# Kernel optimization log

Measured on AMD Instinct MI355X. Metric: run time of the kernel, lower is better.

Reference implementation:

```python
import jax, jax.numpy as jnp
import numpy as np

SCALES = [2 ** i for i in range(11)]  # init: scales=10 -> [1,2,...,1024]
B, N, C, K = 8, 1024, 256, 4096


def setup_inputs() -> dict:
    key = jax.random.key(0)
    k1, k2, k3 = jax.random.split(key, 3)
    f_BNC = jax.random.normal(k1, (B, N, C), dtype=jnp.float32)
    base = jax.random.normal(k2, (K, C), dtype=jnp.float32)          # orthogonal-init codebook base
    proj_w = jax.random.normal(k3, (C, C), dtype=jnp.float32) / np.float32(np.sqrt(C))  # xavier-ish
    proj_b = jnp.zeros((C,), dtype=jnp.float32)
    return {"f_BNC": f_BNC, "base": base, "proj_w": proj_w, "proj_b": proj_b}


def _linear_interp(x, out_size):
    # x: [B, C, n] -> [B, C, out_size], matches F.interpolate(mode='linear', align_corners=False)
    n = x.shape[-1]
    scale = n / out_size
    src = jnp.maximum((jnp.arange(out_size, dtype=jnp.float32) + 0.5) * scale - 0.5, 0.0)
    i0 = jnp.floor(src).astype(jnp.int32)
    i1 = jnp.minimum(i0 + 1, n - 1)
    w = (src - i0.astype(jnp.float32)).astype(x.dtype)
    return x[..., i0] * (1.0 - w) + x[..., i1] * w


def reference(f_BNC, base, proj_w, proj_b):
    sg = jax.lax.stop_gradient
    # update_embedding(): embedding = proj(base)
    embedding = base @ proj_w.T + proj_b                 # [K, C]
    emb_ng = sg(embedding)
    e_sq = jnp.sum(emb_ng * emb_ng, axis=1)              # [K]

    f_BCN = jnp.transpose(f_BNC, (0, 2, 1))              # [B, C, N]
    f_ng = sg(f_BCN)
    f_rest = f_ng
    f_hat = jnp.zeros_like(f_ng)
    commit = jnp.float32(0.0)
    qlat = jnp.float32(0.0)
    SN = len(SCALES)

    for pn in SCALES:
        # area interpolation == exact mean pooling since N % pn == 0
        rest_BCp = f_rest.reshape(B, C, pn, N // pn).mean(axis=-1)       # [B, C, pn]
        q = jnp.transpose(rest_BCp, (0, 2, 1)).reshape(-1, C)            # [B*pn, C]
        # squared-distance to codebook (gradients never flow through d: argmin only)
        d = jnp.sum(q * q, axis=1, keepdims=True) + e_sq - 2.0 * (q @ emb_ng.T)  # [B*pn, K]
        idx = jnp.argmin(d, axis=1)                                      # [B*pn]
        h_BnC = embedding[idx].reshape(B, pn, C)                         # gather (grad flows to codebook)
        h_BCn = _linear_interp(jnp.transpose(h_BnC, (0, 2, 1)), N)       # [B, C, N]
        f_hat = f_hat + h_BCn
        # residual feeds only argmin at the next scale -> dead gradient path in torch too
        f_rest = f_rest - sg(h_BCn)
        commit = commit + 0.25 * jnp.mean((sg(f_hat) - f_BCN) ** 2)
        qlat = qlat + jnp.mean((f_hat - f_ng) ** 2)

    commit = commit / SN
    qlat = qlat / SN
    # straight-through: f_hat = (f_hat.data - f_no_grad) + f_BCN
    f_out = sg(f_hat) - f_ng + f_BCN
    return (jnp.transpose(f_out, (0, 2, 1)), commit, qlat)
```

## Files before the change

### kernel.cpp

```cpp
#include <hip/hip_runtime.h>
#include <cfloat>

#define BB 8
#define NN 1024
#define CC 256
#define KK 4096
#define SN 11
#define BNC (BB*NN*CC)
#define RMAX 8192

typedef __attribute__((ext_vector_type(8))) _Float16 half8;
typedef __attribute__((ext_vector_type(4))) float f32x4;

__device__ __forceinline__ void split2(float v, ushort& h, ushort& l) {
    union { _Float16 f; ushort u; } a, b;
    a.f = (_Float16)v;
    b.f = (_Float16)(v - (float)a.f);
    h = a.u; l = b.u;
}

__global__ void transpose_pw(const float* __restrict__ pw, float* __restrict__ pwT) {
    int j = blockIdx.x;
    int c = threadIdx.x;
    pwT[j * CC + c] = pw[c * CC + j];
}

__global__ __launch_bounds__(256) void embed_kernel(
    const float* __restrict__ base, const float* __restrict__ pwT,
    const float* __restrict__ pb, float* __restrict__ emb,
    ushort* __restrict__ eh, ushort* __restrict__ el, float* __restrict__ esq) {
    __shared__ float bs[16][CC];
    __shared__ float wpart[16][4];
    int k0 = blockIdx.x * 16;
    int t = threadIdx.x;
    int w = t >> 6, lane = t & 63;
    for (int i = t; i < 16 * CC; i += 256) bs[i >> 8][i & 255] = base[k0 * CC + i];
    __syncthreads();
    float acc[16];
#pragma unroll
    for (int m = 0; m < 16; ++m) acc[m] = 0.f;
    for (int j = 0; j < CC; ++j) {
        float wv = pwT[j * CC + t];
#pragma unroll
        for (int m = 0; m < 16; ++m) acc[m] += bs[m][j] * wv;
    }
    float bias = pb[t];
#pragma unroll
    for (int m = 0; m < 16; ++m) {
        float v = acc[m] + bias;
        int o = (k0 + m) * CC + t;
        emb[o] = v;
        ushort h, l;
        split2(64.f * v, h, l);
        eh[o] = h; el[o] = l;
        float sq = v * v;
#pragma unroll
        for (int d = 1; d < 64; d <<= 1) sq += __shfl_xor(sq, d);
        if (lane == 0) wpart[m][w] = sq;
    }
    __syncthreads();
    if (t < 16) esq[k0 + t] = wpart[t][0] + wpart[t][1] + wpart[t][2] + wpart[t][3];
}

__global__ __launch_bounds__(256) void init_pool16(const float* __restrict__ f,
                                                   float* __restrict__ p16) {
    int blk = blockIdx.x;
    int t = threadIdx.x;
    int c4 = t & 63;
    const float4* src = (const float4*)(f + (size_t)blk * 16 * CC) + c4;
    float4 s = make_float4(0.f, 0.f, 0.f, 0.f);
#pragma unroll
    for (int j = 0; j < 16; ++j) {
        float4 v = src[(size_t)j * 64];
        s.x += v.x; s.y += v.y; s.z += v.z; s.w += v.w;
    }
    ((float4*)(p16 + (size_t)blk * CC))[c4] = s;
}

__global__ __launch_bounds__(256, 4) void dist_small(
    const float* __restrict__ src, const float* __restrict__ emb,
    const float* __restrict__ esq, int R, int g16, int pn, float inv,
    float* __restrict__ pval, int* __restrict__ pidx) {
    __shared__ float qs[32][CC];
    __shared__ float es[64][33];
    int t = threadIdx.x;
    int ws = t >> 6, j = t & 63;
    int k0 = blockIdx.x * 64;
    int r0c = blockIdx.y * 32;
    {
        int row = t >> 3;
        int f4b = (t & 7) * 8;
        int gr = r0c + row;
        float4 a4[8];
#pragma unroll
        for (int ii = 0; ii < 8; ++ii) a4[ii] = make_float4(0.f, 0.f, 0.f, 0.f);
        if (gr < R) {
            int b = gr / pn, p = gr - b * pn;
            const float4* sp = (const float4*)(src + ((size_t)b * 64 + (size_t)p * g16) * CC) + f4b;
            for (int i = 0; i < g16; ++i) {
#pragma unroll
                for (int ii = 0; ii < 8; ++ii) {
                    float4 v = sp[ii];
                    a4[ii].x += v.x; a4[ii].y += v.y; a4[ii].z += v.z; a4[ii].w += v.w;
                }
                sp += 64;
            }
        }
#pragma unroll
        for (int ii = 0; ii < 8; ++ii) {
            a4[ii].x *= inv; a4[ii].y *= inv; a4[ii].z *= inv; a4[ii].w *= inv;
            *(float4*)&qs[row][(f4b + ii) * 4] = a4[ii];
        }
    }
    float acc[8];
#pragma unroll
    for (int ri = 0; ri < 8; ++ri) acc[ri] = 0.f;
    for (int ck = 0; ck < 8; ++ck) {
        __syncthreads();
        {
            int code = t >> 2, cb = (t & 3) * 8;
            float4 v0 = *(const float4*)&emb[(size_t)(k0 + code) * CC + ck * 32 + cb];
            float4 v1 = *(const float4*)&emb[(size_t)(k0 + code) * CC + ck * 32 + cb + 4];
            es[code][cb + 0] = v0.x; es[code][cb + 1] = v0.y;
            es[code][cb + 2] = v0.z; es[code][cb + 3] = v0.w;
            es[code][cb + 4] = v1.x; es[code][cb + 5] = v1.y;
            es[code][cb + 6] = v1.z; es[code][cb + 7] = v1.w;
        }
        __syncthreads();
        for (int c = 0; c < 32; ++c) {
            float ev = es[j][c];
#pragma unroll
            for (int ri = 0; ri < 8; ++ri)
                acc[ri] += qs[ws + 4 * ri][ck * 32 + c] * ev;
        }
    }
    float esv = esq[k0 + j];
#pragma unroll
    for (int ri = 0; ri < 8; ++ri) {
        int r = r0c + ws + 4 * ri;
        if (r >= R) continue;
        float v = esv - 2.f * acc[ri];
        int bi = k0 + j;
#pragma unroll
        for (int d = 1; d < 64; d <<= 1) {
            float ov = __shfl_xor(v, d);
            int oi = __shfl_xor(bi, d);
            if (ov < v || (ov == v && oi < bi)) { v = ov; bi = oi; }
        }
        if (j == 0) {
            pval[(size_t)r * 64 + blockIdx.x] = v;
            pidx[(size_t)r * 64 + blockIdx.x] = bi;
        }
    }
}

__global__ __launch_bounds__(256, 2) void dist_mfma(
    const ushort* __restrict__ qh, const ushort* __restrict__ ql,
    const ushort* __restrict__ eh, const ushort* __restrict__ el,
    const float* __restrict__ esq,
    float* __restrict__ pval, int* __restrict__ pidx) {
    __shared__ ushort tiles[4096 * 8];
    __shared__ float wv[2][128];
    __shared__ int wi[2][128];
    int t = threadIdx.x;
    int w = t >> 6, lane = t & 63;
    int l15 = lane & 15, hi = lane >> 4;
    int wr = w >> 1, wc = w & 1;
    int r0 = blockIdx.x * 128;
    int kb = blockIdx.y;
    int k0 = kb * 128;

    f32x4 acc[4][4];
#pragma unroll
    for (int mi = 0; mi < 4; ++mi)
#pragma unroll
        for (int ni = 0; ni < 4; ++ni) acc[mi][ni] = (f32x4){0.f, 0.f, 0.f, 0.f};

    for (int ck = 0; ck < 4; ++ck) {
        __syncthreads();
#pragma unroll
        for (int it = 0; it < 16; ++it) {
            int s = it * 256 + t;
            const ushort* g;
            if (s < 2048) {
                int a = s >> 10;
                int rem = s & 1023;
                int row = rem >> 3, sr = rem & 7;
                int c = (ck << 6) + ((sr ^ (row & 7)) << 3);
                g = (a ? ql : qh) + (size_t)(r0 + row) * CC + c;
            } else {
                int s2 = s - 2048;
                int b = s2 >> 10;
                int rem = s2 & 1023;
                int kcol = rem >> 3, sr = rem & 7;
                int c = (ck << 6) + ((sr ^ (kcol & 7)) << 3);
                g = (b ? el : eh) + (size_t)(k0 + kcol) * CC + c;
            }
            ushort* lb = &tiles[(size_t)(it * 256 + (w << 6)) * 8];
            __builtin_amdgcn_global_load_lds(
                (const __attribute__((address_space(1))) unsigned int*)g,
                (__attribute__((address_space(3))) unsigned int*)lb, 16, 0, 0);
        }
        __syncthreads();

#pragma unroll
        for (int kk = 0; kk < 2; ++kk) {
            int cs = (kk << 2) + hi;
            half8 bf0[4], bf1[4], af[4];
#pragma unroll
            for (int ni = 0; ni < 4; ++ni) {
                int kcol = (wc << 6) + (ni << 4) + l15;
                int sb = 2048 + (kcol << 3) + (cs ^ (kcol & 7));
                bf0[ni] = *(const half8*)&tiles[sb * 8];
                bf1[ni] = *(const half8*)&tiles[(sb + 1024) * 8];
            }
#pragma unroll
            for (int mi = 0; mi < 4; ++mi) {
                int row = (wr << 6) + (mi << 4) + l15;
                af[mi] = *(const half8*)&tiles[((row << 3) + (cs ^ (row & 7))) * 8];
            }
#pragma unroll
            for (int mi = 0; mi < 4; ++mi)
#pragma unroll
                for (int ni = 0; ni < 4; ++ni)
                    acc[mi][ni] = __builtin_amdgcn_mfma_f32_16x16x32_f16(af[mi], bf0[ni], acc[mi][ni], 0, 0, 0);
#pragma unroll
            for (int mi = 0; mi < 4; ++mi)
#pragma unroll
                for (int ni = 0; ni < 4; ++ni)
                    acc[mi][ni] = __builtin_amdgcn_mfma_f32_16x16x32_f16(af[mi], bf1[ni], acc[mi][ni], 0, 0, 0);
#pragma unroll
            for (int mi = 0; mi < 4; ++mi) {
                int row = (wr << 6) + (mi << 4) + l15;
                af[mi] = *(const half8*)&tiles[(1024 + (row << 3) + (cs ^ (row & 7))) * 8];
            }
#pragma unroll
            for (int mi = 0; mi < 4; ++mi)
#pragma unroll
                for (int ni = 0; ni < 4; ++ni)
                    acc[mi][ni] = __builtin_amdgcn_mfma_f32_16x16x32_f16(af[mi], bf0[ni], acc[mi][ni], 0, 0, 0);
        }
    }

    int cbase = k0 + (wc << 6) + l15;
    float es4[4];
#pragma unroll
    for (int ni = 0; ni < 4; ++ni) es4[ni] = 4096.f * esq[cbase + ni * 16];
#pragma unroll
    for (int mi = 0; mi < 4; ++mi) {
#pragma unroll
        for (int reg = 0; reg < 4; ++reg) {
            float v = es4[0] - 2.f * acc[mi][0][reg];
            int i = cbase;
#pragma unroll
            for (int ni = 1; ni < 4; ++ni) {
                float v1 = es4[ni] - 2.f * acc[mi][ni][reg];
                if (v1 < v) { v = v1; i = cbase + ni * 16; }
            }
#pragma unroll
            for (int d = 1; d < 16; d <<= 1) {
                float ov = __shfl_xor(v, d);
                int oi = __shfl_xor(i, d);
                if (ov < v || (ov == v && oi < i)) { v = ov; i = oi; }
            }
            if (l15 == 0) {
                int row = (wr << 6) + (mi << 4) + (hi << 2) + reg;
                wv[wc][row] = v;
                wi[wc][row] = i;
            }
        }
    }
    __syncthreads();
    if (t < 128) {
        float v = wv[0][t];
        int i = wi[0][t];
        float ov = wv[1][t];
        int oi = wi[1][t];
        if (ov < v || (ov == v && oi < i)) { v = ov; i = oi; }
        pval[(size_t)(r0 + t) * 64 + kb] = v;
        pidx[(size_t)(r0 + t) * 64 + kb] = i;
    }
}

__global__ __launch_bounds__(256) void update_pool(
    const float* __restrict__ emb, const float* __restrict__ pval,
    const int* __restrict__ pidx, const float* __restrict__ rin,
    float* __restrict__ rout, const float* __restrict__ f,
    float* __restrict__ outp, float* __restrict__ parts,
    ushort* __restrict__ qh, ushort* __restrict__ ql,
    float* __restrict__ qf, float* __restrict__ p16u,
    int pn, int gn, int pnn, int ks, int finalflag) {
    int blk = blockIdx.x;
    int b = blk >> 6, n16 = blk & 63;
    int t = threadIdx.x;
    int w = t >> 6, lane = t & 63;
    int n0 = n16 * 16;
    const float scale = (float)pn * (1.0f / 1024.0f);
    float s_lo = (n0 + 0.5f) * scale - 0.5f;
    if (s_lo < 0.f) s_lo = 0.f;
    int r_lo = (int)s_lo;
    float s_hi = (n0 + 15.5f) * scale - 0.5f;
    if (s_hi < 0.f) s_hi = 0.f;
    int r_hi = min((int)s_hi + 1, pn - 1);
    int cnt = r_hi - r_lo + 1;
    __shared__ int sidx[20];
    for (int ri = w; ri < cnt; ri += 4) {
        size_t rowg = (size_t)(b * pn + r_lo + ri) * 64;
        float v = (lane < ks) ? pval[rowg + lane] : FLT_MAX;
        int i = (lane < ks) ? pidx[rowg + lane] : 0x7fffffff;
#pragma unroll
        for (int d = 1; d < 64; d <<= 1) {
            float ov = __shfl_xor(v, d);
            int oi = __shfl_xor(i, d);
            if (ov < v || (ov == v && oi < i)) { v = ov; i = oi; }
        }
        if (lane == 0) sidx[ri] = i;
    }
    __syncthreads();
    __shared__ float4 rlds[16][64];
    __shared__ float wred[4];
    int nsub = t >> 6;
    int c4 = t & 63;
    float sq = 0.f;
#pragma unroll
    for (int jj = 0; jj < 4; ++jj) {
        int j = nsub + 4 * jj;
        int n = n0 + j;
        float s = (n + 0.5f) * scale - 0.5f;
        if (s < 0.f) s = 0.f;
        int i0 = (int)s;
        float wgt = s - (float)i0;
        int i1 = min(i0 + 1, pn - 1);
        int k0 = sidx[i0 - r_lo];
        int k1 = sidx[i1 - r_lo];
        float4 e0 = ((const float4*)(emb + (size_t)k0 * CC))[c4];
        float4 e1 = ((const float4*)(emb + (size_t)k1 * CC))[c4];
        float wm = 1.f - wgt;
        float4 h = make_float4(wm * e0.x + wgt * e1.x, wm * e0.y + wgt * e1.y,
                               wm * e0.z + wgt * e1.z, wm * e0.w + wgt * e1.w);
        size_t o4 = ((size_t)b * NN + n) * 64 + c4;
        float4 rv0 = ((const float4*)rin)[o4];
        float4 rv = make_float4(rv0.x - h.x, rv0.y - h.y, rv0.z - h.z, rv0.w - h.w);
        if (!finalflag) {
            ((float4*)rout)[o4] = rv;
        } else {
            float4 fv = ((const float4*)f)[o4];
            ((float4*)outp)[o4] = make_float4(fv.x - rv.x, fv.y - rv.y,
                                              fv.z - rv.z, fv.w - rv.w);
        }
        sq += rv.x * rv.x + rv.y * rv.y + rv.z * rv.z + rv.w * rv.w;
        rlds[j][c4] = rv;
    }
    for (int off = 32; off > 0; off >>= 1) sq += __shfl_down(sq, off);
    if (lane == 0) wred[w] = sq;
    __syncthreads();
    if (t == 0) parts[blk] = wred[0] + wred[1] + wred[2] + wred[3];
    if (gn == 0) return;
    const float* rl = (const float*)rlds;
    if (gn < 16) {
        float pr = 0.f;
        for (int j = 0; j < 16; ++j) {
            pr += rl[j * CC + t];
            if ((j & (gn - 1)) == (gn - 1)) {
                float mean = pr * (1.f / (float)gn);
                ushort H, L;
                split2(64.f * mean, H, L);
                size_t r = (size_t)b * pnn + (size_t)((n0 + j) / gn);
                qh[r * CC + t] = H;
                ql[r * CC + t] = L;
                pr = 0.f;
            }
        }
    } else {
        float pr = 0.f;
        for (int j = 0; j < 16; ++j) pr += rl[j * CC + t];
        if (gn == 16) qf[(size_t)blk * CC + t] = pr * (1.f / 16.f);
        else p16u[(size_t)blk * CC + t] = pr;
    }
}

__global__ void reduce_final(const float* __restrict__ parts, float* __restrict__ out) {
    __shared__ float red[256];
    int t = threadIdx.x;
    float s = 0.f;
    for (int i = t; i < SN * 512; i += 256) s += parts[i];
    red[t] = s;
    __syncthreads();
    for (int k = 128; k > 0; k >>= 1) {
        if (t < k) red[t] += red[t + k];
        __syncthreads();
    }
    if (t == 0) {
        float mean_sum = red[0] / (float)BNC;
        out[BNC] = 0.25f * mean_sum / (float)SN;
        out[BNC + 1] = mean_sum / (float)SN;
    }
}

extern "C" void kernel_launch(void* const* d_in, const int* in_sizes, int n_in,
                              void* d_out, int out_size, void* d_ws, size_t ws_size,
                              hipStream_t stream) {
    const float* f    = (const float*)d_in[0];
    const float* base = (const float*)d_in[1];
    const float* pw   = (const float*)d_in[2];
    const float* pb   = (const float*)d_in[3];
    float* out = (float*)d_out;

    float* emb   = (float*)d_ws;
    float* esq   = emb + (size_t)KK * CC;
    float* pwT   = esq + KK;
    float* parts = pwT + (size_t)CC * CC;
    float* pval  = parts + (size_t)SN * 512;
    float* p16   = pval + (size_t)RMAX * 64;
    float* p16u  = p16 + (size_t)BB * 64 * CC;
    float* qf    = p16u + (size_t)BB * 64 * CC;
    float* resid = qf + (size_t)512 * CC;
    int*   pidx  = (int*)(resid + BNC);
    ushort* eh = (ushort*)(pidx + (size_t)RMAX * 64);
    ushort* el = eh + (size_t)KK * CC;
    ushort* qh = el + (size_t)KK * CC;
    ushort* ql = qh + (size_t)RMAX * CC;

    transpose_pw<<<CC, CC, 0, stream>>>(pw, pwT);
    embed_kernel<<<KK / 16, 256, 0, stream>>>(base, pwT, pb, emb, eh, el, esq);
    init_pool16<<<BB * 64, 256, 0, stream>>>(f, p16);

    for (int sidx = 0; sidx < SN; ++sidx) {
        int pn = 1 << sidx;
        int R = BB * pn;
        int ks;
        if (pn <= 64) {
            const float* src;
            float inv;
            int g16;
            if (pn == 64)      { src = qf;   g16 = 1;       inv = 1.f; }
            else if (pn == 1)  { src = p16;  g16 = 64;      inv = 1.f / 1024.f; }
            else               { src = p16u; g16 = 64 / pn; inv = 1.f / (16.f * (64 / pn)); }
            dim3 grid(64, (R + 31) / 32);
            dist_small<<<grid, 256, 0, stream>>>(src, emb, esq, R, g16, pn, inv, pval, pidx);
            ks = 64;
        } else {
            dist_mfma<<<dim3(R / 128, 32), 256, 0, stream>>>(qh, ql, eh, el, esq, pval, pidx);
            ks = 32;
        }
        int pnn = (sidx < SN - 1) ? (pn << 1) : 0;
        int gn = pnn ? (NN / pnn) : 0;
        const float* rin = (sidx == 0) ? f : resid;
        update_pool<<<BB * 64, 256, 0, stream>>>(emb, pval, pidx, rin, resid, f, out,
                                                 parts + (size_t)sidx * 512,
                                                 qh, ql, qf, p16u, pn, gn, pnn, ks,
                                                 (sidx == SN - 1) ? 1 : 0);
    }
    reduce_final<<<1, 256, 0, stream>>>(parts, out);
}
```

Measured before the change: 560.3 us.

## Fuse all stages into one persistent kernel with software grid barriers

Replaces about two dozen separate kernel launches (embedding, pooling, the per-scale distance and update kernels, and the final reduction) with a single persistent kernel of 512 blocks. Stages are separated by a global atomic-counter barrier, and each stage's tiles are spread over the blocks with grid-stride loops. The goal is to remove per-launch overhead and the gaps between kernels. In exchange it depends on all 512 blocks being resident at once (at two blocks per CU), uses a shared LDS union sized for the largest stage, and leaves some blocks idle in stages with little work.

```diff
diff --git a/kernel.cpp b/kernel.cpp
--- a/kernel.cpp
+++ b/kernel.cpp
@@ -8,6 +8,7 @@
 #define SN 11
 #define BNC (BB*NN*CC)
 #define RMAX 8192
+#define NBLK 512
 
 typedef __attribute__((ext_vector_type(8))) _Float16 half8;
 typedef __attribute__((ext_vector_type(4))) float f32x4;
@@ -19,381 +20,406 @@
     h = a.u; l = b.u;
 }
 
+__device__ __forceinline__ void gbar(unsigned* cnt, unsigned target) {
+    __syncthreads();
+    if (threadIdx.x == 0) {
+        __threadfence();
+        atomicAdd(cnt, 1u);
+        while (atomicAdd(cnt, 0u) < target) __builtin_amdgcn_s_sleep(4);
+        __threadfence();
+    }
+    __syncthreads();
+}
+
+struct SMm { ushort tiles[4096 * 8]; float wv[2][128]; int wi[2][128]; };
+struct SMs { float qs[32][CC]; float es[64][33]; };
+struct SMe { float bs[16][CC]; float wpart[16][4]; };
+struct SMu { float4 rlds[16][64]; int sel[20]; float wred[4]; };
+struct SMr { float red[256]; };
+union SMem { SMm m; SMs s; SMe e; SMu u; SMr r; };
+
 __global__ void transpose_pw(const float* __restrict__ pw, float* __restrict__ pwT) {
     int j = blockIdx.x;
     int c = threadIdx.x;
     pwT[j * CC + c] = pw[c * CC + j];
 }
 
-__global__ __launch_bounds__(256) void embed_kernel(
-    const float* __restrict__ base, const float* __restrict__ pwT,
-    const float* __restrict__ pb, float* __restrict__ emb,
-    ushort* __restrict__ eh, ushort* __restrict__ el, float* __restrict__ esq) {
-    __shared__ float bs[16][CC];
-    __shared__ float wpart[16][4];
-    int k0 = blockIdx.x * 16;
-    int t = threadIdx.x;
-    int w = t >> 6, lane = t & 63;
-    for (int i = t; i < 16 * CC; i += 256) bs[i >> 8][i & 255] = base[k0 * CC + i];
-    __syncthreads();
-    float acc[16];
-#pragma unroll
-    for (int m = 0; m < 16; ++m) acc[m] = 0.f;
-    for (int j = 0; j < CC; ++j) {
-        float wv = pwT[j * CC + t];
-#pragma unroll
-        for (int m = 0; m < 16; ++m) acc[m] += bs[m][j] * wv;
+__global__ __launch_bounds__(256, 2) void mega(
+    const float* __restrict__ f, const float* __restrict__ base,
+    const float* __restrict__ pwT, const float* __restrict__ pb,
+    float* __restrict__ out,
+    float* __restrict__ emb, float* __restrict__ esq,
+    float* __restrict__ parts, float* __restrict__ pval, int* __restrict__ pidx,
+    float* __restrict__ p16, float* __restrict__ p16u, float* __restrict__ qf,
+    float* __restrict__ resid,
+    ushort* __restrict__ eh, ushort* __restrict__ el,
+    ushort* __restrict__ qh, ushort* __restrict__ ql,
+    unsigned* __restrict__ cnt) {
+    __shared__ SMem sm;
+    const int blk = blockIdx.x;
+    const int t = threadIdx.x;
+    const int w = t >> 6, lane = t & 63;
+    unsigned bph = 0;
+
+    if (blk < 256) {
+        int k0 = blk * 16;
+        for (int i = t; i < 16 * CC; i += 256) sm.e.bs[i >> 8][i & 255] = base[k0 * CC + i];
+        __syncthreads();
+        float acc[16];
+#pragma unroll
+        for (int m = 0; m < 16; ++m) acc[m] = 0.f;
+        for (int j = 0; j < CC; ++j) {
+            float wgt = pwT[j * CC + t];
+#pragma unroll
+            for (int m = 0; m < 16; ++m) acc[m] += sm.e.bs[m][j] * wgt;
+        }
+        float bias = pb[t];
+#pragma unroll
+        for (int m = 0; m < 16; ++m) {
+            float v = acc[m] + bias;
+            int o = (k0 + m) * CC + t;
+            emb[o] = v;
+            ushort h, l;
+            split2(64.f * v, h, l);
+            eh[o] = h; el[o] = l;
+            float sq = v * v;
+#pragma unroll
+            for (int d = 1; d < 64; d <<= 1) sq += __shfl_xor(sq, d);
+            if (lane == 0) sm.e.wpart[m][w] = sq;
+        }
+        __syncthreads();
+        if (t < 16) esq[k0 + t] = sm.e.wpart[t][0] + sm.e.wpart[t][1] +
+                                  sm.e.wpart[t][2] + sm.e.wpart[t][3];
+    } else {
+        for (int bb = blk - 256; bb < 512; bb += 256) {
+            int c4 = t & 63;
+            const float4* src = (const float4*)(f + (size_t)bb * 16 * CC) + c4;
+            float4 s = make_float4(0.f, 0.f, 0.f, 0.f);
+#pragma unroll
+            for (int j = 0; j < 16; ++j) {
+                float4 v = src[(size_t)j * 64];
+                s.x += v.x; s.y += v.y; s.z += v.z; s.w += v.w;
+            }
+            ((float4*)(p16 + (size_t)bb * CC))[c4] = s;
+        }
     }
-    float bias = pb[t];
-#pragma unroll
-    for (int m = 0; m < 16; ++m) {
-        float v = acc[m] + bias;
-        int o = (k0 + m) * CC + t;
-        emb[o] = v;
-        ushort h, l;
-        split2(64.f * v, h, l);
-        eh[o] = h; el[o] = l;
-        float sq = v * v;
-#pragma unroll
-        for (int d = 1; d < 64; d <<= 1) sq += __shfl_xor(sq, d);
-        if (lane == 0) wpart[m][w] = sq;
+    gbar(cnt, (++bph) * NBLK);
+
+    for (int sc = 0; sc < SN; ++sc) {
+        int pn = 1 << sc;
+        int R = BB * pn;
+        int ks;
+        if (pn <= 64) {
+            ks = 64;
+            const float* src;
+            float inv;
+            int g16;
+            if (pn == 64)      { src = qf;   g16 = 1;       inv = 1.f; }
+            else if (pn == 1)  { src = p16;  g16 = 64;      inv = 1.f / 1024.f; }
+            else               { src = p16u; g16 = 64 / pn; inv = 1.f / (16.f * (64 / pn)); }
+            int rch = (R + 31) / 32;
+            int ntile = 64 * rch;
+            for (int tile = blk; tile < ntile; tile += NBLK) {
+                __syncthreads();
+                int kbx = tile & 63, rc = tile >> 6;
+                int k0 = kbx * 64;
+                int r0c = rc * 32;
+                int ws = w, j = lane;
+                {
+                    int row = t >> 3;
+                    int f4b = (t & 7) * 8;
+                    int gr = r0c + row;
+                    float4 a4[8];
+#pragma unroll
+                    for (int ii = 0; ii < 8; ++ii) a4[ii] = make_float4(0.f, 0.f, 0.f, 0.f);
+                    if (gr < R) {
+                        int b = gr / pn, p = gr - b * pn;
+                        const float4* sp = (const float4*)(src + ((size_t)b * 64 + (size_t)p * g16) * CC) + f4b;
+                        for (int i = 0; i < g16; ++i) {
+#pragma unroll
+                            for (int ii = 0; ii < 8; ++ii) {
+                                float4 v = sp[ii];
+                                a4[ii].x += v.x; a4[ii].y += v.y; a4[ii].z += v.z; a4[ii].w += v.w;
+                            }
+                            sp += 64;
+                        }
+                    }
+#pragma unroll
+                    for (int ii = 0; ii < 8; ++ii) {
+                        a4[ii].x *= inv; a4[ii].y *= inv; a4[ii].z *= inv; a4[ii].w *= inv;
+                        *(float4*)&sm.s.qs[row][(f4b + ii) * 4] = a4[ii];
+                    }
+                }
+                float acc[8];
+#pragma unroll
+                for (int ri = 0; ri < 8; ++ri) acc[ri] = 0.f;
+                for (int ck = 0; ck < 8; ++ck) {
+                    __syncthreads();
+                    {
+                        int code = t >> 2, cb = (t & 3) * 8;
+                        float4 v0 = *(const float4*)&emb[(size_t)(k0 + code) * CC + ck * 32 + cb];
+                        float4 v1 = *(const float4*)&emb[(size_t)(k0 + code) * CC + ck * 32 + cb + 4];
+                        sm.s.es[code][cb + 0] = v0.x; sm.s.es[code][cb + 1] = v0.y;
+                        sm.s.es[code][cb + 2] = v0.z; sm.s.es[code][cb + 3] = v0.w;
+                        sm.s.es[code][cb + 4] = v1.x; sm.s.es[code][cb + 5] = v1.y;
+                        sm.s.es[code][cb + 6] = v1.z; sm.s.es[code][cb + 7] = v1.w;
+                    }
+                    __syncthreads();
+                    for (int c = 0; c < 32; ++c) {
+                        float ev = sm.s.es[j][c];
+#pragma unroll
+                        for (int ri = 0; ri < 8; ++ri)
+                            acc[ri] += sm.s.qs[ws + 4 * ri][ck * 32 + c] * ev;
+                    }
+                }
+                float esv = esq[k0 + j];
+#pragma unroll
+                for (int ri = 0; ri < 8; ++ri) {
+                    int r = r0c + ws + 4 * ri;
+                    if (r >= R) continue;
+                    float v = esv - 2.f * acc[ri];
+                    int bi = k0 + j;
+#pragma unroll
+                    for (int d = 1; d < 64; d <<= 1) {
+                        float ov = __shfl_xor(v, d);
+                        int oi = __shfl_xor(bi, d);
+                        if (ov < v || (ov == v && oi < bi)) { v = ov; bi = oi; }
+                    }
+                    if (j == 0) {
+                        pval[(size_t)r * 64 + kbx] = v;
+                        pidx[(size_t)r * 64 + kbx] = bi;
+                    }
+                }
+            }
+        } else {
+            ks = 32;
+            int rb = R >> 7;
+            int ntile = rb << 5;
+            for (int tile = blk; tile < ntile; tile += NBLK) {
+                int rblk = tile & (rb - 1);
+                int kb = tile / rb;
+                int l15 = lane & 15, hi = lane >> 4;
+                int wr = w >> 1, wc = w & 1;
+                int r0 = rblk * 128;
+                int k0 = kb * 128;
+                f32x4 acc[4][4];
+#pragma unroll
+                for (int mi = 0; mi < 4; ++mi)
+#pragma unroll
+                    for (int ni = 0; ni < 4; ++ni) acc[mi][ni] = (f32x4){0.f, 0.f, 0.f, 0.f};
+
+                for (int ck = 0; ck < 4; ++ck) {
+                    __syncthreads();
+#pragma unroll
+                    for (int it = 0; it < 16; ++it) {
+                        int s = it * 256 + t;
+                        const ushort* g;
+                        if (s < 2048) {
+                            int a = s >> 10;
+                            int rem = s & 1023;
+                            int row = rem >> 3, sr = rem & 7;
+                            int c = (ck << 6) + ((sr ^ (row & 7)) << 3);
+                            g = (a ? ql : qh) + (size_t)(r0 + row) * CC + c;
+                        } else {
+                            int s2 = s - 2048;
+                            int b = s2 >> 10;
+                            int rem = s2 & 1023;
+                            int kcol = rem >> 3, sr = rem & 7;
+                            int c = (ck << 6) + ((sr ^ (kcol & 7)) << 3);
+                            g = (b ? el : eh) + (size_t)(k0 + kcol) * CC + c;
+                        }
+                        ushort* lb = &sm.m.tiles[(size_t)(it * 256 + (w << 6)) * 8];
+                        __builtin_amdgcn_global_load_lds(
+                            (const __attribute__((address_space(1))) unsigned int*)g,
+                            (__attribute__((address_space(3))) unsigned int*)lb, 16, 0, 0);
+                    }
+                    __syncthreads();
+#pragma unroll
+                    for (int kk = 0; kk < 2; ++kk) {
+                        int cs = (kk << 2) + hi;
+                        half8 bf0[4], bf1[4], af[4];
+#pragma unroll
+                        for (int ni = 0; ni < 4; ++ni) {
+                            int kcol = (wc << 6) + (ni << 4) + l15;
+                            int sb = 2048 + (kcol << 3) + (cs ^ (kcol & 7));
+                            bf0[ni] = *(const half8*)&sm.m.tiles[sb * 8];
+                            bf1[ni] = *(const half8*)&sm.m.tiles[(sb + 1024) * 8];
+                        }
+#pragma unroll
+                        for (int mi = 0; mi < 4; ++mi) {
+                            int row = (wr << 6) + (mi << 4) + l15;
+                            af[mi] = *(const half8*)&sm.m.tiles[((row << 3) + (cs ^ (row & 7))) * 8];
+                        }
+#pragma unroll
+                        for (int mi = 0; mi < 4; ++mi)
+#pragma unroll
+                            for (int ni = 0; ni < 4; ++ni)
+                                acc[mi][ni] = __builtin_amdgcn_mfma_f32_16x16x32_f16(af[mi], bf0[ni], acc[mi][ni], 0, 0, 0);
+#pragma unroll
+                        for (int mi = 0; mi < 4; ++mi)
+#pragma unroll
+                            for (int ni = 0; ni < 4; ++ni)
+                                acc[mi][ni] = __builtin_amdgcn_mfma_f32_16x16x32_f16(af[mi], bf1[ni], acc[mi][ni], 0, 0, 0);
+#pragma unroll
+                        for (int mi = 0; mi < 4; ++mi) {
+                            int row = (wr << 6) + (mi << 4) + l15;
+                            af[mi] = *(const half8*)&sm.m.tiles[(1024 + (row << 3) + (cs ^ (row & 7))) * 8];
+                        }
+#pragma unroll
+                        for (int mi = 0; mi < 4; ++mi)
+#pragma unroll
+                            for (int ni = 0; ni < 4; ++ni)
+                                acc[mi][ni] = __builtin_amdgcn_mfma_f32_16x16x32_f16(af[mi], bf0[ni], acc[mi][ni], 0, 0, 0);
+                    }
+                }
+                int cbase = k0 + (wc << 6) + l15;
+                float es4[4];
+#pragma unroll
+                for (int ni = 0; ni < 4; ++ni) es4[ni] = 4096.f * esq[cbase + ni * 16];
+#pragma unroll
+                for (int mi = 0; mi < 4; ++mi) {
+#pragma unroll
+                    for (int reg = 0; reg < 4; ++reg) {
+                        float v = es4[0] - 2.f * acc[mi][0][reg];
+                        int i = cbase;
+#pragma unroll
+                        for (int ni = 1; ni < 4; ++ni) {
+                            float v1 = es4[ni] - 2.f * acc[mi][ni][reg];
+                            if (v1 < v) { v = v1; i = cbase + ni * 16; }
+                        }
+#pragma unroll
+                        for (int d = 1; d < 16; d <<= 1) {
+                            float ov = __shfl_xor(v, d);
+                            int oi = __shfl_xor(i, d);
+                            if (ov < v || (ov == v && oi < i)) { v = ov; i = oi; }
+                        }
+                        if (l15 == 0) {
+                            int row = (wr << 6) + (mi << 4) + (hi << 2) + reg;
+                            sm.m.wv[wc][row] = v;
+                            sm.m.wi[wc][row] = i;
+                        }
+                    }
+                }
+                __syncthreads();
+                if (t < 128) {
+                    float v = sm.m.wv[0][t];
+                    int i = sm.m.wi[0][t];
+                    float ov = sm.m.wv[1][t];
+                    int oi = sm.m.wi[1][t];
+                    if (ov < v || (ov == v && oi < i)) { v = ov; i = oi; }
+                    pval[(size_t)(r0 + t) * 64 + kb] = v;
+                    pidx[(size_t)(r0 + t) * 64 + kb] = i;
+                }
+            }
+        }
+        gbar(cnt, (++bph) * NBLK);
+
+        {
+            int pnn = (sc < SN - 1) ? (pn << 1) : 0;
+            int gn = pnn ? (NN / pnn) : 0;
+            int finalflag = (sc == SN - 1) ? 1 : 0;
+            const float* rin = (sc == 0) ? f : resid;
+            float* partsw = parts + (size_t)sc * 512;
+            int b = blk >> 6, n16 = blk & 63;
+            int n0 = n16 * 16;
+            const float scale = (float)pn * (1.0f / 1024.0f);
+            float s_lo = (n0 + 0.5f) * scale - 0.5f;
+            if (s_lo < 0.f) s_lo = 0.f;
+            int r_lo = (int)s_lo;
+            float s_hi = (n0 + 15.5f) * scale - 0.5f;
+            if (s_hi < 0.f) s_hi = 0.f;
+            int r_hi = min((int)s_hi + 1, pn - 1);
+            int cnt2 = r_hi - r_lo + 1;
+            for (int ri = w; ri < cnt2; ri += 4) {
+                size_t rowg = (size_t)(b * pn + r_lo + ri) * 64;
+                float v = (lane < ks) ? pval[rowg + lane] : FLT_MAX;
+                int i = (lane < ks) ? pidx[rowg + lane] : 0x7fffffff;
+#pragma unroll
+                for (int d = 1; d < 64; d <<= 1) {
+                    float ov = __shfl_xor(v, d);
+                    int oi = __shfl_xor(i, d);
+                    if (ov < v || (ov == v && oi < i)) { v = ov; i = oi; }
+                }
+                if (lane == 0) sm.u.sel[ri] = i;
+            }
+            __syncthreads();
+            int nsub = t >> 6;
+            int c4 = t & 63;
+            float sq = 0.f;
+#pragma unroll
+            for (int jj = 0; jj < 4; ++jj) {
+                int j = nsub + 4 * jj;
+                int n = n0 + j;
+                float s = (n + 0.5f) * scale - 0.5f;
+                if (s < 0.f) s = 0.f;
+                int i0 = (int)s;
+                float wgt = s - (float)i0;
+                int i1 = min(i0 + 1, pn - 1);
+                int k0 = sm.u.sel[i0 - r_lo];
+                int k1 = sm.u.sel[i1 - r_lo];
+                float4 e0 = ((const float4*)(emb + (size_t)k0 * CC))[c4];
+                float4 e1 = ((const float4*)(emb + (size_t)k1 * CC))[c4];
+                float wm = 1.f - wgt;
+                float4 h = make_float4(wm * e0.x + wgt * e1.x, wm * e0.y + wgt * e1.y,
+                                       wm * e0.z + wgt * e1.z, wm * e0.w + wgt * e1.w);
+                size_t o4 = ((size_t)b * NN + n) * 64 + c4;
+                float4 rv0 = ((const float4*)rin)[o4];
+                float4 rv = make_float4(rv0.x - h.x, rv0.y - h.y, rv0.z - h.z, rv0.w - h.w);
+                if (!finalflag) {
+                    ((float4*)resid)[o4] = rv;
+                } else {
+                    float4 fv = ((const float4*)f)[o4];
+                    ((float4*)out)[o4] = make_float4(fv.x - rv.x, fv.y - rv.y,
+                                                     fv.z - rv.z, fv.w - rv.w);
+                }
+                sq += rv.x * rv.x + rv.y * rv.y + rv.z * rv.z + rv.w * rv.w;
+                sm.u.rlds[j][c4] = rv;
+            }
+            for (int off = 32; off > 0; off >>= 1) sq += __shfl_down(sq, off);
+            if (lane == 0) sm.u.wred[w] = sq;
+            __syncthreads();
+            if (t == 0) partsw[blk] = sm.u.wred[0] + sm.u.wred[1] + sm.u.wred[2] + sm.u.wred[3];
+            if (gn > 0) {
+                const float* rl = (const float*)sm.u.rlds;
+                if (gn < 16) {
+                    float pr = 0.f;
+                    for (int j = 0; j < 16; ++j) {
+                        pr += rl[j * CC + t];
+                        if ((j & (gn - 1)) == (gn - 1)) {
+                            float mean = pr * (1.f / (float)gn);
+                            ushort H, L;
+                            split2(64.f * mean, H, L);
+                            size_t r = (size_t)b * pnn + (size_t)((n0 + j) / gn);
+                            qh[r * CC + t] = H;
+                            ql[r * CC + t] = L;
+                            pr = 0.f;
+                        }
+                    }
+                } else {
+                    float pr = 0.f;
+                    for (int j = 0; j < 16; ++j) pr += rl[j * CC + t];
+                    if (gn == 16) qf[(size_t)blk * CC + t] = pr * (1.f / 16.f);
+                    else p16u[(size_t)blk * CC + t] = pr;
+                }
+            }
+        }
+        gbar(cnt, (++bph) * NBLK);
     }
-    __syncthreads();
-    if (t < 16) esq[k0 + t] = wpart[t][0] + wpart[t][1] + wpart[t][2] + wpart[t][3];
-}
-
-__global__ __launch_bounds__(256) void init_pool16(const float* __restrict__ f,
-                                                   float* __restrict__ p16) {
-    int blk = blockIdx.x;
-    int t = threadIdx.x;
-    int c4 = t & 63;
-    const float4* src = (const float4*)(f + (size_t)blk * 16 * CC) + c4;
-    float4 s = make_float4(0.f, 0.f, 0.f, 0.f);
-#pragma unroll
-    for (int j = 0; j < 16; ++j) {
-        float4 v = src[(size_t)j * 64];
-        s.x += v.x; s.y += v.y; s.z += v.z; s.w += v.w;
-    }
-    ((float4*)(p16 + (size_t)blk * CC))[c4] = s;
-}
-
-__global__ __launch_bounds__(256, 4) void dist_small(
-    const float* __restrict__ src, const float* __restrict__ emb,
-    const float* __restrict__ esq, int R, int g16, int pn, float inv,
-    float* __restrict__ pval, int* __restrict__ pidx) {
-    __shared__ float qs[32][CC];
-    __shared__ float es[64][33];
-    int t = threadIdx.x;
-    int ws = t >> 6, j = t & 63;
-    int k0 = blockIdx.x * 64;
-    int r0c = blockIdx.y * 32;
-    {
-        int row = t >> 3;
-        int f4b = (t & 7) * 8;
-        int gr = r0c + row;
-        float4 a4[8];
-#pragma unroll
-        for (int ii = 0; ii < 8; ++ii) a4[ii] = make_float4(0.f, 0.f, 0.f, 0.f);
-        if (gr < R) {
-            int b = gr / pn, p = gr - b * pn;
-            const float4* sp = (const float4*)(src + ((size_t)b * 64 + (size_t)p * g16) * CC) + f4b;
-            for (int i = 0; i < g16; ++i) {
-#pragma unroll
-                for (int ii = 0; ii < 8; ++ii) {
-                    float4 v = sp[ii];
-                    a4[ii].x += v.x; a4[ii].y += v.y; a4[ii].z += v.z; a4[ii].w += v.w;
-                }
-                sp += 64;
-            }
-        }
-#pragma unroll
-        for (int ii = 0; ii < 8; ++ii) {
-            a4[ii].x *= inv; a4[ii].y *= inv; a4[ii].z *= inv; a4[ii].w *= inv;
-            *(float4*)&qs[row][(f4b + ii) * 4] = a4[ii];
-        }
-    }
-    float acc[8];
-#pragma unroll
-    for (int ri = 0; ri < 8; ++ri) acc[ri] = 0.f;
-    for (int ck = 0; ck < 8; ++ck) {
+
+    if (blk == 0) {
+        float s = 0.f;
+        for (int i = t; i < SN * 512; i += 256) s += parts[i];
+        sm.r.red[t] = s;
         __syncthreads();
-        {
-            int code = t >> 2, cb = (t & 3) * 8;
-            float4 v0 = *(const float4*)&emb[(size_t)(k0 + code) * CC + ck * 32 + cb];
-            float4 v1 = *(const float4*)&emb[(size_t)(k0 + code) * CC + ck * 32 + cb + 4];
-            es[code][cb + 0] = v0.x; es[code][cb + 1] = v0.y;
-            es[code][cb + 2] = v0.z; es[code][cb + 3] = v0.w;
-            es[code][cb + 4] = v1.x; es[code][cb + 5] = v1.y;
-            es[code][cb + 6] = v1.z; es[code][cb + 7] = v1.w;
-        }
-        __syncthreads();
-        for (int c = 0; c < 32; ++c) {
-            float ev = es[j][c];
-#pragma unroll
-            for (int ri = 0; ri < 8; ++ri)
-                acc[ri] += qs[ws + 4 * ri][ck * 32 + c] * ev;
-        }
-    }
-    float esv = esq[k0 + j];
-#pragma unroll
-    for (int ri = 0; ri < 8; ++ri) {
-        int r = r0c + ws + 4 * ri;
-        if (r >= R) continue;
-        float v = esv - 2.f * acc[ri];
-        int bi = k0 + j;
-#pragma unroll
-        for (int d = 1; d < 64; d <<= 1) {
-            float ov = __shfl_xor(v, d);
-            int oi = __shfl_xor(bi, d);
-            if (ov < v || (ov == v && oi < bi)) { v = ov; bi = oi; }
-        }
-        if (j == 0) {
-            pval[(size_t)r * 64 + blockIdx.x] = v;
-            pidx[(size_t)r * 64 + blockIdx.x] = bi;
-        }
-    }
-}
-
-__global__ __launch_bounds__(256, 2) void dist_mfma(
-    const ushort* __restrict__ qh, const ushort* __restrict__ ql,
-    const ushort* __restrict__ eh, const ushort* __restrict__ el,
-    const float* __restrict__ esq,
-    float* __restrict__ pval, int* __restrict__ pidx) {
-    __shared__ ushort tiles[4096 * 8];
-    __shared__ float wv[2][128];
-    __shared__ int wi[2][128];
-    int t = threadIdx.x;
-    int w = t >> 6, lane = t & 63;
-    int l15 = lane & 15, hi = lane >> 4;
-    int wr = w >> 1, wc = w & 1;
-    int r0 = blockIdx.x * 128;
-    int kb = blockIdx.y;
-    int k0 = kb * 128;
-
-    f32x4 acc[4][4];
-#pragma unroll
-    for (int mi = 0; mi < 4; ++mi)
-#pragma unroll
-        for (int ni = 0; ni < 4; ++ni) acc[mi][ni] = (f32x4){0.f, 0.f, 0.f, 0.f};
-
-    for (int ck = 0; ck < 4; ++ck) {
-        __syncthreads();
-#pragma unroll
-        for (int it = 0; it < 16; ++it) {
-            int s = it * 256 + t;
-            const ushort* g;
-            if (s < 2048) {
-                int a = s >> 10;
-                int rem = s & 1023;
-                int row = rem >> 3, sr = rem & 7;
-                int c = (ck << 6) + ((sr ^ (row & 7)) << 3);
-                g = (a ? ql : qh) + (size_t)(r0 + row) * CC + c;
-            } else {
-                int s2 = s - 2048;
-                int b = s2 >> 10;
-                int rem = s2 & 1023;
-                int kcol = rem >> 3, sr = rem & 7;
-                int c = (ck << 6) + ((sr ^ (kcol & 7)) << 3);
-                g = (b ? el : eh) + (size_t)(k0 + kcol) * CC + c;
-            }
-            ushort* lb = &tiles[(size_t)(it * 256 + (w << 6)) * 8];
-            __builtin_amdgcn_global_load_lds(
-                (const __attribute__((address_space(1))) unsigned int*)g,
-                (__attribute__((address_space(3))) unsigned int*)lb, 16, 0, 0);
-        }
-        __syncthreads();
-
-#pragma unroll
-        for (int kk = 0; kk < 2; ++kk) {
-            int cs = (kk << 2) + hi;
-            half8 bf0[4], bf1[4], af[4];
-#pragma unroll
-            for (int ni = 0; ni < 4; ++ni) {
-                int kcol = (wc << 6) + (ni << 4) + l15;
-                int sb = 2048 + (kcol << 3) + (cs ^ (kcol & 7));
-                bf0[ni] = *(const half8*)&tiles[sb * 8];
-                bf1[ni] = *(const half8*)&tiles[(sb + 1024) * 8];
-            }
-#pragma unroll
-            for (int mi = 0; mi < 4; ++mi) {
-                int row = (wr << 6) + (mi << 4) + l15;
-                af[mi] = *(const half8*)&tiles[((row << 3) + (cs ^ (row & 7))) * 8];
-            }
-#pragma unroll
-            for (int mi = 0; mi < 4; ++mi)
-#pragma unroll
-                for (int ni = 0; ni < 4; ++ni)
-                    acc[mi][ni] = __builtin_amdgcn_mfma_f32_16x16x32_f16(af[mi], bf0[ni], acc[mi][ni], 0, 0, 0);
-#pragma unroll
-            for (int mi = 0; mi < 4; ++mi)
-#pragma unroll
-                for (int ni = 0; ni < 4; ++ni)
-                    acc[mi][ni] = __builtin_amdgcn_mfma_f32_16x16x32_f16(af[mi], bf1[ni], acc[mi][ni], 0, 0, 0);
-#pragma unroll
-            for (int mi = 0; mi < 4; ++mi) {
-                int row = (wr << 6) + (mi << 4) + l15;
-                af[mi] = *(const half8*)&tiles[(1024 + (row << 3) + (cs ^ (row & 7))) * 8];
-            }
-#pragma unroll
-            for (int mi = 0; mi < 4; ++mi)
-#pragma unroll
-                for (int ni = 0; ni < 4; ++ni)
-                    acc[mi][ni] = __builtin_amdgcn_mfma_f32_16x16x32_f16(af[mi], bf0[ni], acc[mi][ni], 0, 0, 0);
-        }
-    }
-
-    int cbase = k0 + (wc << 6) + l15;
-    float es4[4];
-#pragma unroll
-    for (int ni = 0; ni < 4; ++ni) es4[ni] = 4096.f * esq[cbase + ni * 16];
-#pragma unroll
-    for (int mi = 0; mi < 4; ++mi) {
-#pragma unroll
-        for (int reg = 0; reg < 4; ++reg) {
-            float v = es4[0] - 2.f * acc[mi][0][reg];
-            int i = cbase;
-#pragma unroll
-            for (int ni = 1; ni < 4; ++ni) {
-                float v1 = es4[ni] - 2.f * acc[mi][ni][reg];
-                if (v1 < v) { v = v1; i = cbase + ni * 16; }
-            }
-#pragma unroll
-            for (int d = 1; d < 16; d <<= 1) {
-                float ov = __shfl_xor(v, d);
-                int oi = __shfl_xor(i, d);
-                if (ov < v || (ov == v && oi < i)) { v = ov; i = oi; }
-            }
-            if (l15 == 0) {
-                int row = (wr << 6) + (mi << 4) + (hi << 2) + reg;
-                wv[wc][row] = v;
-                wi[wc][row] = i;
-            }
-        }
-    }
-    __syncthreads();
-    if (t < 128) {
-        float v = wv[0][t];
-        int i = wi[0][t];
-        float ov = wv[1][t];
-        int oi = wi[1][t];
-        if (ov < v || (ov == v && oi < i)) { v = ov; i = oi; }
-        pval[(size_t)(r0 + t) * 64 + kb] = v;
-        pidx[(size_t)(r0 + t) * 64 + kb] = i;
-    }
-}
-
-__global__ __launch_bounds__(256) void update_pool(
-    const float* __restrict__ emb, const float* __restrict__ pval,
-    const int* __restrict__ pidx, const float* __restrict__ rin,
-    float* __restrict__ rout, const float* __restrict__ f,
-    float* __restrict__ outp, float* __restrict__ parts,
-    ushort* __restrict__ qh, ushort* __restrict__ ql,
-    float* __restrict__ qf, float* __restrict__ p16u,
-    int pn, int gn, int pnn, int ks, int finalflag) {
-    int blk = blockIdx.x;
-    int b = blk >> 6, n16 = blk & 63;
-    int t = threadIdx.x;
-    int w = t >> 6, lane = t & 63;
-    int n0 = n16 * 16;
-    const float scale = (float)pn * (1.0f / 1024.0f);
-    float s_lo = (n0 + 0.5f) * scale - 0.5f;
-    if (s_lo < 0.f) s_lo = 0.f;
-    int r_lo = (int)s_lo;
-    float s_hi = (n0 + 15.5f) * scale - 0.5f;
-    if (s_hi < 0.f) s_hi = 0.f;
-    int r_hi = min((int)s_hi + 1, pn - 1);
-    int cnt = r_hi - r_lo + 1;
-    __shared__ int sidx[20];
-    for (int ri = w; ri < cnt; ri += 4) {
-        size_t rowg = (size_t)(b * pn + r_lo + ri) * 64;
-        float v = (lane < ks) ? pval[rowg + lane] : FLT_MAX;
-        int i = (lane < ks) ? pidx[rowg + lane] : 0x7fffffff;
-#pragma unroll
-        for (int d = 1; d < 64; d <<= 1) {
-            float ov = __shfl_xor(v, d);
-            int oi = __shfl_xor(i, d);
-            if (ov < v || (ov == v && oi < i)) { v = ov; i = oi; }
-        }
-        if (lane == 0) sidx[ri] = i;
-    }
-    __syncthreads();
-    __shared__ float4 rlds[16][64];
-    __shared__ float wred[4];
-    int nsub = t >> 6;
-    int c4 = t & 63;
-    float sq = 0.f;
-#pragma unroll
-    for (int jj = 0; jj < 4; ++jj) {
-        int j = nsub + 4 * jj;
-        int n = n0 + j;
-        float s = (n + 0.5f) * scale - 0.5f;
-        if (s < 0.f) s = 0.f;
-        int i0 = (int)s;
-        float wgt = s - (float)i0;
-        int i1 = min(i0 + 1, pn - 1);
-        int k0 = sidx[i0 - r_lo];
-        int k1 = sidx[i1 - r_lo];
-        float4 e0 = ((const float4*)(emb + (size_t)k0 * CC))[c4];
-        float4 e1 = ((const float4*)(emb + (size_t)k1 * CC))[c4];
-        float wm = 1.f - wgt;
-        float4 h = make_float4(wm * e0.x + wgt * e1.x, wm * e0.y + wgt * e1.y,
-                               wm * e0.z + wgt * e1.z, wm * e0.w + wgt * e1.w);
-        size_t o4 = ((size_t)b * NN + n) * 64 + c4;
-        float4 rv0 = ((const float4*)rin)[o4];
-        float4 rv = make_float4(rv0.x - h.x, rv0.y - h.y, rv0.z - h.z, rv0.w - h.w);
-        if (!finalflag) {
-            ((float4*)rout)[o4] = rv;
-        } else {
-            float4 fv = ((const float4*)f)[o4];
-            ((float4*)outp)[o4] = make_float4(fv.x - rv.x, fv.y - rv.y,
-                                              fv.z - rv.z, fv.w - rv.w);
-        }
-        sq += rv.x * rv.x + rv.y * rv.y + rv.z * rv.z + rv.w * rv.w;
-        rlds[j][c4] = rv;
-    }
-    for (int off = 32; off > 0; off >>= 1) sq += __shfl_down(sq, off);
-    if (lane == 0) wred[w] = sq;
-    __syncthreads();
-    if (t == 0) parts[blk] = wred[0] + wred[1] + wred[2] + wred[3];
-    if (gn == 0) return;
-    const float* rl = (const float*)rlds;
-    if (gn < 16) {
-        float pr = 0.f;
-        for (int j = 0; j < 16; ++j) {
-            pr += rl[j * CC + t];
-            if ((j & (gn - 1)) == (gn - 1)) {
-                float mean = pr * (1.f / (float)gn);
-                ushort H, L;
-                split2(64.f * mean, H, L);
-                size_t r = (size_t)b * pnn + (size_t)((n0 + j) / gn);
-                qh[r * CC + t] = H;
-                ql[r * CC + t] = L;
-                pr = 0.f;
-            }
-        }
-    } else {
-        float pr = 0.f;
-        for (int j = 0; j < 16; ++j) pr += rl[j * CC + t];
-        if (gn == 16) qf[(size_t)blk * CC + t] = pr * (1.f / 16.f);
-        else p16u[(size_t)blk * CC + t] = pr;
-    }
-}
-
-__global__ void reduce_final(const float* __restrict__ parts, float* __restrict__ out) {
-    __shared__ float red[256];
-    int t = threadIdx.x;
-    float s = 0.f;
-    for (int i = t; i < SN * 512; i += 256) s += parts[i];
-    red[t] = s;
-    __syncthreads();
-    for (int k = 128; k > 0; k >>= 1) {
-        if (t < k) red[t] += red[t + k];
-        __syncthreads();
-    }
-    if (t == 0) {
-        float mean_sum = red[0] / (float)BNC;
-        out[BNC] = 0.25f * mean_sum / (float)SN;
-        out[BNC + 1] = mean_sum / (float)SN;
+        for (int k = 128; k > 0; k >>= 1) {
+            if (t < k) sm.r.red[t] += sm.r.red[t + k];
+            __syncthreads();
+        }
+        if (t == 0) {
+            float mean_sum = sm.r.red[0] / (float)BNC;
+            out[BNC] = 0.25f * mean_sum / (float)SN;
+            out[BNC + 1] = mean_sum / (float)SN;
+        }
     }
 }
 
@@ -420,36 +446,12 @@
     ushort* el = eh + (size_t)KK * CC;
     ushort* qh = el + (size_t)KK * CC;
     ushort* ql = qh + (size_t)RMAX * CC;
-
+    unsigned* cnt = (unsigned*)(ql + (size_t)RMAX * CC);
+
+    hipMemsetAsync(cnt, 0, 8, stream);
     transpose_pw<<<CC, CC, 0, stream>>>(pw, pwT);
-    embed_kernel<<<KK / 16, 256, 0, stream>>>(base, pwT, pb, emb, eh, el, esq);
-    init_pool16<<<BB * 64, 256, 0, stream>>>(f, p16);
-
-    for (int sidx = 0; sidx < SN; ++sidx) {
-        int pn = 1 << sidx;
-        int R = BB * pn;
-        int ks;
-        if (pn <= 64) {
-            const float* src;
-            float inv;
-            int g16;
-            if (pn == 64)      { src = qf;   g16 = 1;       inv = 1.f; }
-            else if (pn == 1)  { src = p16;  g16 = 64;      inv = 1.f / 1024.f; }
-            else               { src = p16u; g16 = 64 / pn; inv = 1.f / (16.f * (64 / pn)); }
-            dim3 grid(64, (R + 31) / 32);
-            dist_small<<<grid, 256, 0, stream>>>(src, emb, esq, R, g16, pn, inv, pval, pidx);
-            ks = 64;
-        } else {
-            dist_mfma<<<dim3(R / 128, 32), 256, 0, stream>>>(qh, ql, eh, el, esq, pval, pidx);
-            ks = 32;
-        }
-        int pnn = (sidx < SN - 1) ? (pn << 1) : 0;
-        int gn = pnn ? (NN / pnn) : 0;
-        const float* rin = (sidx == 0) ? f : resid;
-        update_pool<<<BB * 64, 256, 0, stream>>>(emb, pval, pidx, rin, resid, f, out,
-                                                 parts + (size_t)sidx * 512,
-                                                 qh, ql, qf, p16u, pn, gn, pnn, ks,
-                                                 (sidx == SN - 1) ? 1 : 0);
-    }
-    reduce_final<<<1, 256, 0, stream>>>(parts, out);
+    mega<<<NBLK, 256, 0, stream>>>(f, base, pwT, pb, out,
+                                   emb, esq, parts, pval, pidx,
+                                   p16, p16u, qf, resid,
+                                   eh, el, qh, ql, cnt);
 }
```

Measured after the change: 1.516 ms. +170.6%, slower.

## Double-buffer MFMA distance tiles and merge prep kernels into one launch

Applied to the files above, without the earlier changes.

The MFMA distance kernel now splits the channel dimension into eight 32-wide chunks held in two LDS buffers. The next chunk is loaded asynchronously while the current one feeds the MFMAs, so global-to-LDS load latency overlaps compute and the two barriers per chunk become one. Separately, the projection-weight transpose and the initial 16-way pooling are fused into a single prep kernel, saving one launch. The smaller swizzle (xor over 4 slots instead of 8) may increase LDS bank conflicts, and the extra loop iterations add some overhead.

```diff
diff --git a/kernel.cpp b/kernel.cpp
--- a/kernel.cpp
+++ b/kernel.cpp
@@ -19,10 +19,26 @@
     h = a.u; l = b.u;
 }
 
-__global__ void transpose_pw(const float* __restrict__ pw, float* __restrict__ pwT) {
-    int j = blockIdx.x;
-    int c = threadIdx.x;
-    pwT[j * CC + c] = pw[c * CC + j];
+__global__ __launch_bounds__(256) void prep_kernel(const float* __restrict__ pw,
+                                                   float* __restrict__ pwT,
+                                                   const float* __restrict__ f,
+                                                   float* __restrict__ p16) {
+    int blk = blockIdx.x;
+    int t = threadIdx.x;
+    if (blk < 256) {
+        pwT[blk * CC + t] = pw[t * CC + blk];
+    } else {
+        int bb = blk - 256;
+        int c4 = t & 63;
+        const float4* src = (const float4*)(f + (size_t)bb * 16 * CC) + c4;
+        float4 s = make_float4(0.f, 0.f, 0.f, 0.f);
+#pragma unroll
+        for (int j = 0; j < 16; ++j) {
+            float4 v = src[(size_t)j * 64];
+            s.x += v.x; s.y += v.y; s.z += v.z; s.w += v.w;
+        }
+        ((float4*)(p16 + (size_t)bb * CC))[c4] = s;
+    }
 }
 
 __global__ __launch_bounds__(256) void embed_kernel(
@@ -60,21 +76,6 @@
     }
     __syncthreads();
     if (t < 16) esq[k0 + t] = wpart[t][0] + wpart[t][1] + wpart[t][2] + wpart[t][3];
-}
-
-__global__ __launch_bounds__(256) void init_pool16(const float* __restrict__ f,
-                                                   float* __restrict__ p16) {
-    int blk = blockIdx.x;
-    int t = threadIdx.x;
-    int c4 = t & 63;
-    const float4* src = (const float4*)(f + (size_t)blk * 16 * CC) + c4;
-    float4 s = make_float4(0.f, 0.f, 0.f, 0.f);
-#pragma unroll
-    for (int j = 0; j < 16; ++j) {
-        float4 v = src[(size_t)j * 64];
-        s.x += v.x; s.y += v.y; s.z += v.z; s.w += v.w;
-    }
-    ((float4*)(p16 + (size_t)blk * CC))[c4] = s;
 }
 
 __global__ __launch_bounds__(256, 4) void dist_small(
@@ -159,7 +160,7 @@
     const ushort* __restrict__ eh, const ushort* __restrict__ el,
     const float* __restrict__ esq,
     float* __restrict__ pval, int* __restrict__ pidx) {
-    __shared__ ushort tiles[4096 * 8];
+    __shared__ ushort tiles[2][2048 * 8];
     __shared__ float wv[2][128];
     __shared__ int wi[2][128];
     int t = threadIdx.x;
@@ -170,76 +171,79 @@
     int kb = blockIdx.y;
     int k0 = kb * 128;
 
-    f32x4 acc[4][4];
-#pragma unroll
-    for (int mi = 0; mi < 4; ++mi)
-#pragma unroll
-        for (int ni = 0; ni < 4; ++ni) acc[mi][ni] = (f32x4){0.f, 0.f, 0.f, 0.f};
-
-    for (int ck = 0; ck < 4; ++ck) {
-        __syncthreads();
-#pragma unroll
-        for (int it = 0; it < 16; ++it) {
+    auto stage = [&](int ck, int bb) {
+#pragma unroll
+        for (int it = 0; it < 8; ++it) {
             int s = it * 256 + t;
             const ushort* g;
-            if (s < 2048) {
-                int a = s >> 10;
-                int rem = s & 1023;
-                int row = rem >> 3, sr = rem & 7;
-                int c = (ck << 6) + ((sr ^ (row & 7)) << 3);
+            if (s < 1024) {
+                int a = s >> 9;
+                int rem = s & 511;
+                int row = rem >> 2, sr = rem & 3;
+                int c = (ck << 5) + ((sr ^ (row & 3)) << 3);
                 g = (a ? ql : qh) + (size_t)(r0 + row) * CC + c;
             } else {
-                int s2 = s - 2048;
-                int b = s2 >> 10;
-                int rem = s2 & 1023;
-                int kcol = rem >> 3, sr = rem & 7;
-                int c = (ck << 6) + ((sr ^ (kcol & 7)) << 3);
-                g = (b ? el : eh) + (size_t)(k0 + kcol) * CC + c;
-            }
-            ushort* lb = &tiles[(size_t)(it * 256 + (w << 6)) * 8];
+                int s2 = s - 1024;
+                int b2 = s2 >> 9;
+                int rem = s2 & 511;
+                int kcol = rem >> 2, sr = rem & 3;
+                int c = (ck << 5) + ((sr ^ (kcol & 3)) << 3);
+                g = (b2 ? el : eh) + (size_t)(k0 + kcol) * CC + c;
+            }
+            ushort* lb = &tiles[bb][(size_t)(it * 256 + (w << 6)) * 8];
             __builtin_amdgcn_global_load_lds(
                 (const __attribute__((address_space(1))) unsigned int*)g,
                 (__attribute__((address_space(3))) unsigned int*)lb, 16, 0, 0);
         }
+    };
+
+    f32x4 acc[4][4];
+#pragma unroll
+    for (int mi = 0; mi < 4; ++mi)
+#pragma unroll
+        for (int ni = 0; ni < 4; ++ni) acc[mi][ni] = (f32x4){0.f, 0.f, 0.f, 0.f};
+
+    stage(0, 0);
+    __syncthreads();
+
+    for (int ck = 0; ck < 8; ++ck) {
+        int cur = ck & 1;
+        if (ck + 1 < 8) stage(ck + 1, cur ^ 1);
+        int cs = hi;
+        half8 bf0[4], bf1[4], af[4];
+#pragma unroll
+        for (int ni = 0; ni < 4; ++ni) {
+            int kcol = (wc << 6) + (ni << 4) + l15;
+            int sb = 1024 + (kcol << 2) + (cs ^ (kcol & 3));
+            bf0[ni] = *(const half8*)&tiles[cur][sb * 8];
+            bf1[ni] = *(const half8*)&tiles[cur][(sb + 512) * 8];
+        }
+#pragma unroll
+        for (int mi = 0; mi < 4; ++mi) {
+            int row = (wr << 6) + (mi << 4) + l15;
+            af[mi] = *(const half8*)&tiles[cur][((row << 2) + (cs ^ (row & 3))) * 8];
+        }
+#pragma unroll
+        for (int mi = 0; mi < 4; ++mi)
+#pragma unroll
+            for (int ni = 0; ni < 4; ++ni)
+                acc[mi][ni] = __builtin_amdgcn_mfma_f32_16x16x32_f16(af[mi], bf0[ni], acc[mi][ni], 0, 0, 0);
+#pragma unroll
+        for (int mi = 0; mi < 4; ++mi)
+#pragma unroll
+            for (int ni = 0; ni < 4; ++ni)
+                acc[mi][ni] = __builtin_amdgcn_mfma_f32_16x16x32_f16(af[mi], bf1[ni], acc[mi][ni], 0, 0, 0);
+#pragma unroll
+        for (int mi = 0; mi < 4; ++mi) {
+            int row = (wr << 6) + (mi << 4) + l15;
+            af[mi] = *(const half8*)&tiles[cur][(512 + (row << 2) + (cs ^ (row & 3))) * 8];
+        }
+#pragma unroll
+        for (int mi = 0; mi < 4; ++mi)
+#pragma unroll
+            for (int ni = 0; ni < 4; ++ni)
+                acc[mi][ni] = __builtin_amdgcn_mfma_f32_16x16x32_f16(af[mi], bf0[ni], acc[mi][ni], 0, 0, 0);
         __syncthreads();
-
-#pragma unroll
-        for (int kk = 0; kk < 2; ++kk) {
-            int cs = (kk << 2) + hi;
-            half8 bf0[4], bf1[4], af[4];
-#pragma unroll
-            for (int ni = 0; ni < 4; ++ni) {
-                int kcol = (wc << 6) + (ni << 4) + l15;
-                int sb = 2048 + (kcol << 3) + (cs ^ (kcol & 7));
-                bf0[ni] = *(const half8*)&tiles[sb * 8];
-                bf1[ni] = *(const half8*)&tiles[(sb + 1024) * 8];
-            }
-#pragma unroll
-            for (int mi = 0; mi < 4; ++mi) {
-                int row = (wr << 6) + (mi << 4) + l15;
-                af[mi] = *(const half8*)&tiles[((row << 3) + (cs ^ (row & 7))) * 8];
-            }
-#pragma unroll
-            for (int mi = 0; mi < 4; ++mi)
-#pragma unroll
-                for (int ni = 0; ni < 4; ++ni)
-                    acc[mi][ni] = __builtin_amdgcn_mfma_f32_16x16x32_f16(af[mi], bf0[ni], acc[mi][ni], 0, 0, 0);
-#pragma unroll
-            for (int mi = 0; mi < 4; ++mi)
-#pragma unroll
-                for (int ni = 0; ni < 4; ++ni)
-                    acc[mi][ni] = __builtin_amdgcn_mfma_f32_16x16x32_f16(af[mi], bf1[ni], acc[mi][ni], 0, 0, 0);
-#pragma unroll
-            for (int mi = 0; mi < 4; ++mi) {
-                int row = (wr << 6) + (mi << 4) + l15;
-                af[mi] = *(const half8*)&tiles[(1024 + (row << 3) + (cs ^ (row & 7))) * 8];
-            }
-#pragma unroll
-            for (int mi = 0; mi < 4; ++mi)
-#pragma unroll
-                for (int ni = 0; ni < 4; ++ni)
-                    acc[mi][ni] = __builtin_amdgcn_mfma_f32_16x16x32_f16(af[mi], bf0[ni], acc[mi][ni], 0, 0, 0);
-        }
     }
 
     int cbase = k0 + (wc << 6) + l15;
@@ -421,9 +425,8 @@
     ushort* qh = el + (size_t)KK * CC;
     ushort* ql = qh + (size_t)RMAX * CC;
 
-    transpose_pw<<<CC, CC, 0, stream>>>(pw, pwT);
+    prep_kernel<<<768, 256, 0, stream>>>(pw, pwT, f, p16);
     embed_kernel<<<KK / 16, 256, 0, stream>>>(base, pwT, pb, emb, eh, el, esq);
-    init_pool16<<<BB * 64, 256, 0, stream>>>(f, p16);
 
     for (int sidx = 0; sidx < SN; ++sidx) {
         int pn = 1 << sidx;
```

New measurement: 776.5 us. 1.39x slower.
